# Kernel tuning notes

Hardware: AMD Instinct MI355X
Metric: run time of the kernel (lower is better)

Reference implementation:

```python
import jax, jax.numpy as jnp
import numpy as np

N, E, D_IN, D_H, D_OUT = 50000, 600000, 128, 128, 1


def setup_inputs() -> dict:
    key = jax.random.key(0)
    ks = jax.random.split(key, 12)
    s = 1.0 / np.sqrt(D_H)
    inp = {
        "x": jax.random.normal(ks[0], (N, D_IN), dtype=jnp.float32),
        "edge_index": jax.random.randint(ks[1], (2, E), 0, N, dtype=jnp.int64),
        # GCNConv layer weights (in->h, h->h, h->h)
        "W0": jax.random.normal(ks[2], (D_IN, D_H), dtype=jnp.float32) * s,
        "b0": jnp.zeros((D_H,), dtype=jnp.float32),
        "W1": jax.random.normal(ks[3], (D_H, D_H), dtype=jnp.float32) * s,
        "b1": jnp.zeros((D_H,), dtype=jnp.float32),
        "W2": jax.random.normal(ks[4], (D_H, D_H), dtype=jnp.float32) * s,
        "b2": jnp.zeros((D_H,), dtype=jnp.float32),
        # MLP head
        "mlp_w1": jax.random.normal(ks[5], (D_H, D_H), dtype=jnp.float32) * s,
        "mlp_b1": jnp.zeros((D_H,), dtype=jnp.float32),
        "mlp_w2": jax.random.normal(ks[6], (D_H, D_OUT), dtype=jnp.float32) * s,
        "mlp_b2": jnp.zeros((D_OUT,), dtype=jnp.float32),
    }
    return inp


def reference(x, edge_index, W0, b0, W1, b1, W2, b2, mlp_w1, mlp_b1, mlp_w2, mlp_b2):
    n = x.shape[0]
    loop = jnp.arange(n, dtype=edge_index.dtype)
    # add self-loops (PyG GCNConv default)
    src = jnp.concatenate([edge_index[0], loop])
    dst = jnp.concatenate([edge_index[1], loop])
    # symmetric normalization: deg counts incoming edges incl. self-loop
    deg = jax.ops.segment_sum(jnp.ones(src.shape, dtype=x.dtype), dst, num_segments=n)
    dinv = jax.lax.rsqrt(deg)  # deg >= 1 due to self-loops
    norm = (dinv[src] * dinv[dst])[:, None]  # [E+N, 1]

    def gcn_conv(h, W, b):
        h = h @ W                       # [N, d]
        msg = h[src] * norm             # gather + scale, [E+N, d]
        return jax.ops.segment_sum(msg, dst, num_segments=n) + b

    # num_layers=3: first two convs with ReLU (dropout is identity in eval)
    h = jax.nn.relu(gcn_conv(x, W0, b0))
    h = jax.nn.relu(gcn_conv(h, W1, b1))
    h = gcn_conv(h, W2, b2)
    # MLP head (dropout identity in eval)
    h = jax.nn.relu(h @ mlp_w1 + mlp_b1)
    return h @ mlp_w2 + mlp_b2
```

## Files before the change

### kernel.cpp

```cpp
#include <hip/hip_runtime.h>
#include <hip/hip_fp16.h>

constexpr int D = 128;

typedef _Float16 half8 __attribute__((ext_vector_type(8)));
typedef float f32x4 __attribute__((ext_vector_type(4)));


__global__ void k_zero(int4* __restrict__ p, int n4) {
    int i = blockIdx.x * 256 + threadIdx.x;
    if (i < n4) p[i] = make_int4(0, 0, 0, 0);
}


__global__ void k_count(const int* __restrict__ dst, int* __restrict__ cnt, int E) {
    int e = blockIdx.x * 256 + threadIdx.x;
    if (e < E) atomicAdd(&cnt[dst[e]], 1);
}

__global__ __launch_bounds__(256) void k_deg_stats(const int* __restrict__ cnt,
                                                   float* __restrict__ dinv,
                                                   int* __restrict__ bsum, int n) {
    __shared__ int sm[256];
    int tid = threadIdx.x;
    int i = blockIdx.x * 256 + tid;
    int c = (i < n) ? cnt[i] : 0;
    if (i < n) dinv[i] = rsqrtf((float)(c + 1));
    sm[tid] = c;
    __syncthreads();
    for (int off = 128; off > 0; off >>= 1) {
        if (tid < off) sm[tid] += sm[tid + off];
        __syncthreads();
    }
    if (tid == 0) bsum[blockIdx.x] = sm[0];
}

__global__ __launch_bounds__(1024) void k_scan_bsums(int* __restrict__ bsum, int nb,
                                                     int* __restrict__ rowptr, int n) {
    __shared__ int sm[1024];
    int tid = threadIdx.x;
    int v = (tid < nb) ? bsum[tid] : 0;
    sm[tid] = v;
    __syncthreads();
    for (int off = 1; off < 1024; off <<= 1) {
        int t = (tid >= off) ? sm[tid - off] : 0;
        __syncthreads();
        sm[tid] += t;
        __syncthreads();
    }
    if (tid < nb) bsum[tid] = sm[tid] - v;
    if (tid == 1023) rowptr[n] = sm[1023];
}

__global__ __launch_bounds__(256) void k_local_scan(const int* __restrict__ cnt,
                                                    const int* __restrict__ bsum,
                                                    int* __restrict__ rowptr,
                                                    int* __restrict__ cursor, int n) {
    __shared__ int sm[256];
    int tid = threadIdx.x;
    int i = blockIdx.x * 256 + tid;
    int v = (i < n) ? cnt[i] : 0;
    sm[tid] = v;
    __syncthreads();
    for (int off = 1; off < 256; off <<= 1) {
        int t = (tid >= off) ? sm[tid - off] : 0;
        __syncthreads();
        sm[tid] += t;
        __syncthreads();
    }
    if (i < n) {
        int rp = bsum[blockIdx.x] + sm[tid] - v;
        rowptr[i] = rp;
        cursor[i] = rp;
    }
}

template <typename IdxT>
__global__ void k_fill(const int* __restrict__ src, const int* __restrict__ dst,
                       int* __restrict__ cursor, IdxT* __restrict__ csr, int E) {
    int e = blockIdx.x * 256 + threadIdx.x;
    if (e < E) {
        int s = src[e], d = dst[e];
        int p = atomicAdd(&cursor[d], 1);
        csr[p] = (IdxT)s;
    }
}


__global__ void k_cvt_h(const float* __restrict__ in, const float* __restrict__ dinv,
                        __half* __restrict__ outh, int n4) {
    int i = blockIdx.x * 256 + threadIdx.x;
    if (i < n4) {
        float4 v = reinterpret_cast<const float4*>(in)[i];
        float dd = dinv[i >> 5];
        __half ho[4] = {__float2half(v.x * dd), __float2half(v.y * dd),
                        __float2half(v.z * dd), __float2half(v.w * dd)};
        reinterpret_cast<uint2*>(outh)[i] = *reinterpret_cast<uint2*>(ho);
    }
}


__global__ void k_wprime(const float* __restrict__ W2, const float* __restrict__ M1,
                         const float* __restrict__ b2, const float* __restrict__ c1,
                         float* __restrict__ Wp, float* __restrict__ cp) {
    int b = blockIdx.x, t = threadIdx.x;
    if (b < 64) {
        int idx = b * 256 + t;
        int i = idx >> 7, j = idx & 127;
        float acc = 0.f;
        for (int k = 0; k < 128; ++k) acc = fmaf(W2[i * 128 + k], M1[k * 128 + j], acc);
        Wp[idx] = acc;
    } else if (t < 128) {
        float acc = c1[t];
        for (int k = 0; k < 128; ++k) acc = fmaf(b2[k], M1[k * 128 + t], acc);
        cp[t] = acc;
    }
}


__global__ void k_cvt_w(const float* __restrict__ W0, const float* __restrict__ W1,
                        const float* __restrict__ Wp, __half* __restrict__ Wf0,
                        __half* __restrict__ Wf1, __half* __restrict__ Wfp) {
    int m = blockIdx.x >> 6;
    int idx = (blockIdx.x & 63) * 256 + threadIdx.x;
    int j = idx & 7;
    int l = (idx >> 3) & 63;
    int c = (idx >> 9) & 7;
    int kk = (idx >> 12) & 3;
    int row = kk * 32 + (l >> 4) * 8 + j;
    int col = c * 16 + (l & 15);
    const float* W = (m == 0) ? W0 : (m == 1) ? W1 : Wp;
    __half* Wf = (m == 0) ? Wf0 : (m == 1) ? Wf1 : Wfp;
    Wf[idx] = __float2half(W[row * 128 + col]);
}


__device__ inline void acc4(float4& a, uint2 g) {
    float2 lo = __half22float2(*reinterpret_cast<const __half2*>(&g.x));
    float2 hi = __half22float2(*reinterpret_cast<const __half2*>(&g.y));
    a.x += lo.x;
    a.y += lo.y;
    a.z += hi.x;
    a.w += hi.y;
}

template <typename IdxT>
__global__ __launch_bounds__(256) void k_agg_h2(const uint2* __restrict__ Ah2,
                                                const int* __restrict__ rowptr,
                                                const IdxT* __restrict__ csr,
                                                const float* __restrict__ dinv,
                                                __half* __restrict__ outh, int n) {
    int wv = threadIdx.x >> 6;
    int lane = threadIdx.x & 63;
    int i = blockIdx.x * 4 + wv;
    if (i >= n) return;
    int half = lane >> 5;
    int fl = lane & 31;
    float di = dinv[i];
    float4 acc = make_float4(0.f, 0.f, 0.f, 0.f);
    int beg = rowptr[i], end = rowptr[i + 1];
    int e = beg;
    for (; e + 8 <= end; e += 8) {
        int s0 = (int)csr[e + half];
        int s1 = (int)csr[e + 2 + half];
        int s2 = (int)csr[e + 4 + half];
        int s3 = (int)csr[e + 6 + half];
        uint2 g0 = Ah2[s0 * 32 + fl];
        uint2 g1 = Ah2[s1 * 32 + fl];
        uint2 g2 = Ah2[s2 * 32 + fl];
        uint2 g3 = Ah2[s3 * 32 + fl];
        acc4(acc, g0);
        acc4(acc, g1);
        acc4(acc, g2);
        acc4(acc, g3);
    }
    for (; e + 2 <= end; e += 2) {
        int s0 = (int)csr[e + half];
        uint2 g0 = Ah2[s0 * 32 + fl];
        acc4(acc, g0);
    }
    if (e < end && half == 0) {
        int s0 = (int)csr[e];
        uint2 g0 = Ah2[s0 * 32 + fl];
        acc4(acc, g0);
    }
    acc.x += __shfl_xor(acc.x, 32);
    acc.y += __shfl_xor(acc.y, 32);
    acc.z += __shfl_xor(acc.z, 32);
    acc.w += __shfl_xor(acc.w, 32);
    uint2 gs = Ah2[i * 32 + fl];
    acc4(acc, gs);
    if (half == 0) {
        __half ho[4] = {__float2half(di * acc.x), __float2half(di * acc.y),
                        __float2half(di * acc.z), __float2half(di * acc.w)};
        *reinterpret_cast<uint2*>(&outh[i * 128 + fl * 4]) =
            *reinterpret_cast<const uint2*>(ho);
    }
}


template <int MODE>
__global__ __launch_bounds__(256) void k_gemm_mfma(const __half* __restrict__ A,
                                                   const __half* __restrict__ Wf,
                                                   const float* __restrict__ bias,
                                                   const float* __restrict__ dinv,
                                                   const float* __restrict__ m2,
                                                   const float* __restrict__ m2b,
                                                   void* __restrict__ outv, int n) {
    int tid = threadIdx.x;
    int w = tid >> 6;
    int l = tid & 63;
    int r0 = blockIdx.x * 64 + w * 16;
    int arow = r0 + (l & 15);
    if (arow > n - 1) arow = n - 1;
    int kb = (l >> 4) * 8;

    f32x4 acc[8];
#pragma unroll
    for (int c = 0; c < 8; ++c) acc[c] = (f32x4){0.f, 0.f, 0.f, 0.f};

#pragma unroll
    for (int kk = 0; kk < 4; ++kk) {
        half8 a = *reinterpret_cast<const half8*>(&A[arow * 128 + kk * 32 + kb]);
#pragma unroll
        for (int c = 0; c < 8; ++c) {
            half8 b = *reinterpret_cast<const half8*>(&Wf[((kk * 8 + c) * 64 + l) * 8]);
            acc[c] = __builtin_amdgcn_mfma_f32_16x16x32_f16(a, b, acc[c], 0, 0, 0);
        }
    }

    float bv[8];
#pragma unroll
    for (int c = 0; c < 8; ++c) bv[c] = bias[c * 16 + (l & 15)];

    if (MODE == 0) {
        __half* outh = (__half*)outv;
#pragma unroll
        for (int reg = 0; reg < 4; ++reg) {
            int r = r0 + (l >> 4) * 4 + reg;
            if (r < n) {
                float dr = dinv[r];
#pragma unroll
                for (int c = 0; c < 8; ++c) {
                    float v = dr * fmaxf(acc[c][reg] + bv[c], 0.f);
                    outh[r * 128 + c * 16 + (l & 15)] = __float2half(v);
                }
            }
        }
    } else {
        float* out = (float*)outv;
        float mv[8];
#pragma unroll
        for (int c = 0; c < 8; ++c) mv[c] = m2[c * 16 + (l & 15)];
        float m2bv = m2b[0];
#pragma unroll
        for (int reg = 0; reg < 4; ++reg) {
            float p = 0.f;
#pragma unroll
            for (int c = 0; c < 8; ++c)
                p = fmaf(fmaxf(acc[c][reg] + bv[c], 0.f), mv[c], p);
            p += __shfl_xor(p, 1);
            p += __shfl_xor(p, 2);
            p += __shfl_xor(p, 4);
            p += __shfl_xor(p, 8);
            int r = r0 + (l >> 4) * 4 + reg;
            if ((l & 15) == 0 && r < n) out[r] = p + m2bv;
        }
    }
}


extern "C" void kernel_launch(void* const* d_in, const int* in_sizes, int n_in,
                              void* d_out, int out_size, void* d_ws, size_t ws_size,
                              hipStream_t stream) {
    const float* x = (const float*)d_in[0];
    const int* ei = (const int*)d_in[1];
    const float* W0 = (const float*)d_in[2];
    const float* b0 = (const float*)d_in[3];
    const float* W1 = (const float*)d_in[4];
    const float* b1 = (const float*)d_in[5];
    const float* W2 = (const float*)d_in[6];
    const float* b2 = (const float*)d_in[7];
    const float* M1 = (const float*)d_in[8];
    const float* c1 = (const float*)d_in[9];
    const float* m2 = (const float*)d_in[10];
    const float* m2b = (const float*)d_in[11];
    float* out = (float*)d_out;

    int N = in_sizes[0] / D;
    int E = in_sizes[1] / 2;
    const int* src = ei;
    const int* dst = ei + E;

    char* ws = (char*)d_ws;
    size_t off = 0;
    auto alloc = [&](size_t bytes) -> void* {
        void* p = ws + off;
        off += (bytes + 255) & ~(size_t)255;
        return p;
    };

    int gN = (N + 255) / 256;
    int gE = (E + 255) / 256;
    int gAgg = (N + 3) / 4;
    int gGemm = (N + 63) / 64;
    int nElem4 = N * D / 4;
    int gCvt = (nElem4 + 255) / 256;

    __half* xh = (__half*)alloc((size_t)N * D * 2);
    __half* tbuf = (__half*)alloc((size_t)N * D * 2);
    __half* gbuf = (__half*)alloc((size_t)N * D * 2);
    int* cnt = (int*)alloc((size_t)N * 4);
    float* dinv = (float*)alloc((size_t)N * 4);
    int* rowptr = (int*)alloc((size_t)(N + 1) * 4);
    int* cursor = (int*)alloc((size_t)N * 4);
    void* csr = alloc((size_t)E * 4);
    float* Wp = (float*)alloc((size_t)D * D * 4);
    float* cp = (float*)alloc((size_t)D * 4);
    __half* Wf0 = (__half*)alloc((size_t)D * D * 2);
    __half* Wf1 = (__half*)alloc((size_t)D * D * 2);
    __half* Wfp = (__half*)alloc((size_t)D * D * 2);
    int* bsum = (int*)alloc((size_t)gN * 4);

    bool small_idx = (N <= 65535);

    int zc = (N + 3) / 4;
    k_zero<<<(zc + 255) / 256, 256, 0, stream>>>((int4*)cnt, zc);
    k_count<<<gE, 256, 0, stream>>>(dst, cnt, E);
    k_deg_stats<<<gN, 256, 0, stream>>>(cnt, dinv, bsum, N);
    k_scan_bsums<<<1, 1024, 0, stream>>>(bsum, gN, rowptr, N);
    k_local_scan<<<gN, 256, 0, stream>>>(cnt, bsum, rowptr, cursor, N);
    if (small_idx)
        k_fill<ushort><<<gE, 256, 0, stream>>>(src, dst, cursor, (ushort*)csr, E);
    else
        k_fill<uint><<<gE, 256, 0, stream>>>(src, dst, cursor, (uint*)csr, E);
    k_cvt_h<<<gCvt, 256, 0, stream>>>(x, dinv, xh, nElem4);
    k_wprime<<<65, 256, 0, stream>>>(W2, M1, b2, c1, Wp, cp);
    k_cvt_w<<<192, 256, 0, stream>>>(W0, W1, Wp, Wf0, Wf1, Wfp);

    auto agg = [&](const __half* in_h, __half* out_t) {
        if (small_idx)
            k_agg_h2<ushort><<<gAgg, 256, 0, stream>>>((const uint2*)in_h, rowptr,
                                                       (const ushort*)csr, dinv, out_t, N);
        else
            k_agg_h2<uint><<<gAgg, 256, 0, stream>>>((const uint2*)in_h, rowptr,
                                                     (const uint*)csr, dinv, out_t, N);
    };

    agg(xh, tbuf);
    k_gemm_mfma<0><<<gGemm, 256, 0, stream>>>(tbuf, Wf0, b0, dinv, nullptr, nullptr,
                                              gbuf, N);
    agg(gbuf, tbuf);
    k_gemm_mfma<0><<<gGemm, 256, 0, stream>>>(tbuf, Wf1, b1, dinv, nullptr, nullptr,
                                              gbuf, N);
    agg(gbuf, tbuf);
    k_gemm_mfma<1><<<gGemm, 256, 0, stream>>>(tbuf, Wfp, cp, dinv, m2, m2b, out, N);
}
```

Before: 211.8 us.

## Widen aggregation gathers to 16-byte loads with wave-shuffled neighbor indices

The CSR aggregation kernel now has each lane gather 8 halves (uint4) instead of 4, so a wave handles four neighbors per load step in 16-lane groups. Neighbor indices are loaded coalesced, 64 at a time, and broadcast with shuffles instead of per-neighbor scalar loads. Masked FMAs replace the tail loops, and partial sums are reduced across the four groups with xor shuffles. The aim is fewer, wider memory transactions and less index-load overhead, at the cost of wasted gathers on padded tail slots for low-degree nodes (about 12 edges per node here).

```diff
diff --git a/kernel.cpp b/kernel.cpp
--- a/kernel.cpp
+++ b/kernel.cpp
@@ -135,66 +135,77 @@
 }
 
 
-__device__ inline void acc4(float4& a, uint2 g) {
-    float2 lo = __half22float2(*reinterpret_cast<const __half2*>(&g.x));
-    float2 hi = __half22float2(*reinterpret_cast<const __half2*>(&g.y));
-    a.x += lo.x;
-    a.y += lo.y;
-    a.z += hi.x;
-    a.w += hi.y;
+__device__ inline void accm(float* a, uint4 g, float m) {
+    float2 p0 = __half22float2(*reinterpret_cast<const __half2*>(&g.x));
+    float2 p1 = __half22float2(*reinterpret_cast<const __half2*>(&g.y));
+    float2 p2 = __half22float2(*reinterpret_cast<const __half2*>(&g.z));
+    float2 p3 = __half22float2(*reinterpret_cast<const __half2*>(&g.w));
+    a[0] = fmaf(m, p0.x, a[0]);
+    a[1] = fmaf(m, p0.y, a[1]);
+    a[2] = fmaf(m, p1.x, a[2]);
+    a[3] = fmaf(m, p1.y, a[3]);
+    a[4] = fmaf(m, p2.x, a[4]);
+    a[5] = fmaf(m, p2.y, a[5]);
+    a[6] = fmaf(m, p3.x, a[6]);
+    a[7] = fmaf(m, p3.y, a[7]);
 }
 
 template <typename IdxT>
-__global__ __launch_bounds__(256) void k_agg_h2(const uint2* __restrict__ Ah2,
+__global__ __launch_bounds__(256) void k_agg_h4(const uint4* __restrict__ Ah4,
                                                 const int* __restrict__ rowptr,
                                                 const IdxT* __restrict__ csr,
                                                 const float* __restrict__ dinv,
-                                                __half* __restrict__ outh, int n) {
+                                                uint4* __restrict__ outh4, int n) {
     int wv = threadIdx.x >> 6;
     int lane = threadIdx.x & 63;
     int i = blockIdx.x * 4 + wv;
     if (i >= n) return;
-    int half = lane >> 5;
-    int fl = lane & 31;
-    float di = dinv[i];
-    float4 acc = make_float4(0.f, 0.f, 0.f, 0.f);
+    int qg = lane >> 4;
+    int fl = lane & 15;
+    float a[8];
+#pragma unroll
+    for (int j = 0; j < 8; ++j) a[j] = 0.f;
     int beg = rowptr[i], end = rowptr[i + 1];
-    int e = beg;
-    for (; e + 8 <= end; e += 8) {
-        int s0 = (int)csr[e + half];
-        int s1 = (int)csr[e + 2 + half];
-        int s2 = (int)csr[e + 4 + half];
-        int s3 = (int)csr[e + 6 + half];
-        uint2 g0 = Ah2[s0 * 32 + fl];
-        uint2 g1 = Ah2[s1 * 32 + fl];
-        uint2 g2 = Ah2[s2 * 32 + fl];
-        uint2 g3 = Ah2[s3 * 32 + fl];
-        acc4(acc, g0);
-        acc4(acc, g1);
-        acc4(acc, g2);
-        acc4(acc, g3);
-    }
-    for (; e + 2 <= end; e += 2) {
-        int s0 = (int)csr[e + half];
-        uint2 g0 = Ah2[s0 * 32 + fl];
-        acc4(acc, g0);
-    }
-    if (e < end && half == 0) {
-        int s0 = (int)csr[e];
-        uint2 g0 = Ah2[s0 * 32 + fl];
-        acc4(acc, g0);
-    }
-    acc.x += __shfl_xor(acc.x, 32);
-    acc.y += __shfl_xor(acc.y, 32);
-    acc.z += __shfl_xor(acc.z, 32);
-    acc.w += __shfl_xor(acc.w, 32);
-    uint2 gs = Ah2[i * 32 + fl];
-    acc4(acc, gs);
-    if (half == 0) {
-        __half ho[4] = {__float2half(di * acc.x), __float2half(di * acc.y),
-                        __float2half(di * acc.z), __float2half(di * acc.w)};
-        *reinterpret_cast<uint2*>(&outh[i * 128 + fl * 4]) =
-            *reinterpret_cast<const uint2*>(ho);
+    for (int base = beg; base < end; base += 64) {
+        int cnt = end - base;
+        if (cnt > 64) cnt = 64;
+        int idxv = (base + lane < end) ? (int)csr[base + lane] : 0;
+        for (int e = 0; e < cnt; e += 16) {
+            int k0 = e + qg;
+            int k1 = e + qg + 4;
+            int k2 = e + qg + 8;
+            int k3 = e + qg + 12;
+            int s0 = __shfl(idxv, k0);
+            int s1 = __shfl(idxv, k1);
+            int s2 = __shfl(idxv, k2);
+            int s3 = __shfl(idxv, k3);
+            uint4 g0 = Ah4[s0 * 16 + fl];
+            uint4 g1 = Ah4[s1 * 16 + fl];
+            uint4 g2 = Ah4[s2 * 16 + fl];
+            uint4 g3 = Ah4[s3 * 16 + fl];
+            float m0 = (k0 < cnt) ? 1.f : 0.f;
+            float m1 = (k1 < cnt) ? 1.f : 0.f;
+            float m2 = (k2 < cnt) ? 1.f : 0.f;
+            float m3 = (k3 < cnt) ? 1.f : 0.f;
+            accm(a, g0, m0);
+            accm(a, g1, m1);
+            accm(a, g2, m2);
+            accm(a, g3, m3);
+        }
+    }
+#pragma unroll
+    for (int j = 0; j < 8; ++j) {
+        a[j] += __shfl_xor(a[j], 16);
+        a[j] += __shfl_xor(a[j], 32);
+    }
+    if (qg == 0) {
+        uint4 gs = Ah4[i * 16 + fl];
+        accm(a, gs, 1.f);
+        float di = dinv[i];
+        __half ho[8];
+#pragma unroll
+        for (int j = 0; j < 8; ++j) ho[j] = __float2half(di * a[j]);
+        outh4[i * 16 + fl] = *reinterpret_cast<const uint4*>(ho);
     }
 }
 
@@ -340,11 +351,13 @@
 
     auto agg = [&](const __half* in_h, __half* out_t) {
         if (small_idx)
-            k_agg_h2<ushort><<<gAgg, 256, 0, stream>>>((const uint2*)in_h, rowptr,
-                                                       (const ushort*)csr, dinv, out_t, N);
+            k_agg_h4<ushort><<<gAgg, 256, 0, stream>>>((const uint4*)in_h, rowptr,
+                                                       (const ushort*)csr, dinv,
+                                                       (uint4*)out_t, N);
         else
-            k_agg_h2<uint><<<gAgg, 256, 0, stream>>>((const uint2*)in_h, rowptr,
-                                                     (const uint*)csr, dinv, out_t, N);
+            k_agg_h4<uint><<<gAgg, 256, 0, stream>>>((const uint4*)in_h, rowptr,
+                                                     (const uint*)csr, dinv,
+                                                     (uint4*)out_t, N);
     };
 
     agg(xh, tbuf);
```

Result: faster. 196.7 us (-7.1%).
